# Performance work log

Measured on AMD Instinct MI355X. Metric: run time of the kernel, lower is better.

Reference implementation:

```python
import jax, jax.numpy as jnp
import numpy as np

N = 32768   # total nodes (128 graphs x 256 nodes)
E = 262144  # total edges (avg degree 8)
B = 128     # graphs per batch
M = 512     # candidate moves per graph
H = 256     # hidden_dim
F = 32      # raw node feature dim (node_feat_dim - 2)
EPS = 1e-5


def setup_inputs() -> dict:
    key = jax.random.key(0)
    ks = jax.random.split(key, 24)
    f32 = jnp.float32

    def w(k, shape, s=0.05):
        return jax.random.normal(k, shape, f32) * s

    inp = {}
    inp["x"] = jax.random.normal(ks[0], (N, F), f32)
    inp["edge_index"] = jax.random.randint(ks[1], (2, E), 0, N)
    inp["move_index"] = jax.random.randint(ks[2], (B, M, 2), 0, N)
    inp["player"] = jax.random.randint(ks[3], (B,), 0, 2)
    inp["batch"] = jnp.arange(N, dtype=jnp.int64 if jax.config.jax_enable_x64 else jnp.int32) // (N // B)

    inp["Win"] = w(ks[4], (F + 2, H)); inp["b_in"] = jnp.zeros((H,), f32)
    inp["Wg1"] = w(ks[5], (H, H)); inp["bg1"] = jnp.zeros((H,), f32)
    inp["Wg2"] = w(ks[6], (H, H)); inp["bg2"] = jnp.zeros((H,), f32)
    inp["Wg3"] = w(ks[7], (H, H)); inp["bg3"] = jnp.zeros((H,), f32)
    for i in (1, 2, 3):
        inp[f"ln{i}_g"] = jnp.ones((H,), f32)
        inp[f"ln{i}_b"] = jnp.zeros((H,), f32)
    inp["Wfc1"] = w(ks[8], (H, H)); inp["bfc1"] = jnp.zeros((H,), f32)
    inp["Wfc2"] = w(ks[9], (H, H)); inp["bfc2"] = jnp.zeros((H,), f32)
    for i in (1, 2):
        inp[f"bn{i}_g"] = jnp.ones((H,), f32)
        inp[f"bn{i}_b"] = jnp.zeros((H,), f32)
        inp[f"bn{i}_m"] = jnp.zeros((H,), f32)  # running mean (eval mode)
        inp[f"bn{i}_v"] = jnp.ones((H,), f32)   # running var  (eval mode)
    inp["Wp1"] = w(ks[10], (2 * H, H)); inp["bp1"] = jnp.zeros((H,), f32)
    inp["Wp2"] = w(ks[11], (H, 1));     inp["bp2"] = jnp.zeros((1,), f32)
    inp["Wv"]  = w(ks[12], (H, 1));     inp["bv"]  = jnp.zeros((1,), f32)
    return inp


def _layernorm(h, g, b):
    m = h.mean(-1, keepdims=True)
    v = ((h - m) ** 2).mean(-1, keepdims=True)
    return (h - m) * jax.lax.rsqrt(v + EPS) * g + b


def _batchnorm_eval(z, g, b, m, v):
    return (z - m) * jax.lax.rsqrt(v + EPS) * g + b


def reference(x, edge_index, move_index, player, batch,
              Win, b_in, Wg1, bg1, Wg2, bg2, Wg3, bg3,
              ln1_g, ln1_b, ln2_g, ln2_b, ln3_g, ln3_b,
              Wfc1, bfc1, Wfc2, bfc2,
              bn1_g, bn1_b, bn1_m, bn1_v, bn2_g, bn2_b, bn2_m, bn2_v,
              Wp1, bp1, Wp2, bp2, Wv, bv):
    nb = player.shape[0]
    src, dst = edge_index[0], edge_index[1]

    # player one-hot broadcast to nodes, concat, input projection
    ph = jax.nn.one_hot(player, 2, dtype=x.dtype)          # [B,2]
    h = jnp.concatenate([x, ph[batch]], axis=1) @ Win + b_in  # [N,H]
    residual = h

    def gin(h, W, b):  # GINConv(eps=0): lin(x + scatter_add of neighbor feats)
        agg = jnp.zeros_like(h).at[dst].add(h[src])
        return (h + agg) @ W + b

    h = jax.nn.relu(_layernorm(gin(h, Wg1, bg1), ln1_g, ln1_b))
    h = jax.nn.relu(_layernorm(gin(h, Wg2, bg2), ln2_g, ln2_b))
    h = _layernorm(gin(h, Wg3, bg3), ln3_g, ln3_b)
    h = jax.nn.relu(h + residual)

    # global mean pool
    sums = jax.ops.segment_sum(h, batch, num_segments=nb)
    cnt = jax.ops.segment_sum(jnp.ones((h.shape[0], 1), h.dtype), batch, num_segments=nb)
    ge = sums / cnt

    # value head (eval mode: BN uses running stats, dropout is identity)
    v1 = jax.nn.relu(_batchnorm_eval(ge @ Wfc1 + bfc1, bn1_g, bn1_b, bn1_m, bn1_v))
    v2 = jax.nn.relu(_batchnorm_eval(v1 @ Wfc2 + bfc2, bn2_g, bn2_b, bn2_m, bn2_v))
    value = jnp.tanh(v2 @ Wv + bv)[:, 0]                    # [B]

    # policy head: gather node pairs, edge MLP, mask invalid moves (vectorized over B)
    valid = jnp.all(move_index != -1, axis=-1)              # [B,M]
    s = jnp.clip(move_index[..., 0], 0, None)
    t = jnp.clip(move_index[..., 1], 0, None)
    ef = jnp.concatenate([h[s], h[t]], axis=-1)             # [B,M,2H]
    logits = (jax.nn.relu(ef @ Wp1 + bp1) @ Wp2 + bp2)[..., 0]
    policy = jnp.where(valid, logits, jnp.asarray(-1e9, h.dtype))
    return policy, value
```

## Files before the change

kernel.cpp:

```cpp
#include <hip/hip_runtime.h>
#include <hip/hip_bf16.h>

#define HD 256
#define NN 32768
#define NE 262144
#define NB 128
#define NM 512
#define KADJ 48

typedef short bf16x8 __attribute__((ext_vector_type(8)));
typedef float f32x4 __attribute__((ext_vector_type(4)));
typedef unsigned short u16;
typedef unsigned short u16x8 __attribute__((ext_vector_type(8)));
typedef unsigned short u16x4 __attribute__((ext_vector_type(4)));

__device__ __forceinline__ float b2f(u16 u) {
    unsigned int i = ((unsigned int)u) << 16;
    float f; __builtin_memcpy(&f, &i, 4); return f;
}
__device__ __forceinline__ u16 f2b(float f) {
    unsigned int i; __builtin_memcpy(&i, &f, 4);
    return (u16)((i + 0x7FFFu + ((i >> 16) & 1u)) >> 16);
}

__global__ __launch_bounds__(256) void k_prep(const float* __restrict__ Wg1, const float* __restrict__ Wg2,
                                              const float* __restrict__ Wg3, const float* __restrict__ Wp1,
                                              u16* __restrict__ Ws1, u16* __restrict__ Ws2,
                                              u16* __restrict__ Ws3, u16* __restrict__ Wsa,
                                              u16* __restrict__ Wsb,
                                              const float* __restrict__ x, const int* __restrict__ player,
                                              const float* __restrict__ Win, const float* __restrict__ bin,
                                              u16* __restrict__ h0,
                                              const int* __restrict__ esrc, const int* __restrict__ edst,
                                              int* __restrict__ deg, int* __restrict__ adj,
                                              u16* __restrict__ p0, u16* __restrict__ p1, u16* __restrict__ p2) {
    __shared__ float smem[64 * 65];
    const int bid = blockIdx.x;
    const int tid = threadIdx.x;
    if (bid < 80) {
        float (*tile)[65] = (float (*)[65])smem;
        const int mid = bid >> 4, tb = bid & 15;
        const float* W; u16* D;
        switch (mid) {
            case 0: W = Wg1; D = Ws1; break;
            case 1: W = Wg2; D = Ws2; break;
            case 2: W = Wg3; D = Ws3; break;
            case 3: W = Wp1; D = Wsa; break;
            default: W = Wp1 + HD * HD; D = Wsb; break;
        }
        const int tk = tb >> 2, tn = tb & 3;
        const int c = tid & 63, r4 = tid >> 6;
#pragma unroll
        for (int r = 0; r < 16; r++) {
            int k = tk * 64 + r * 4 + r4;
            tile[r * 4 + r4][c] = W[(size_t)k * HD + tn * 64 + c];
        }
        __syncthreads();
#pragma unroll
        for (int r = 0; r < 16; r++) {
            int n = tn * 64 + r * 4 + r4;
            int k = tk * 64 + c;
            u16 val = f2b(tile[c][r * 4 + r4]);
            if (mid < 3) {
                int half = k >> 7;
                int c2 = ((k >> 3) & 15) ^ (n & 15);
                D[half * 32768 + n * 128 + c2 * 8 + (k & 7)] = val;
            } else {
                int cc = k >> 3;
                int c2 = (cc & 16) | ((cc & 15) ^ (n & 15));
                D[n * 256 + c2 * 8 + (k & 7)] = val;
            }
        }
    } else if (bid == 80) {
        if (tid < 96) {
            const int r = tid >> 5, c = tid & 31;
            u16* p = (r == 0) ? p0 : (r == 1) ? p1 : p2;
            u16x8 z = (u16x8){0, 0, 0, 0, 0, 0, 0, 0};
            *(u16x8*)(p + c * 8) = z;
        }
    } else if (bid < 337) {
        const int lane = tid & 63, wvv = tid >> 6;
        const int l15 = lane & 15, lg = lane >> 4;
        const int node0 = (bid - 81) * 128;
        const int g = node0 >> 8;
        const int pl = player[g];

        bf16x8 wfr[16];
#pragma unroll
        for (int fc = 0; fc < 16; fc++) {
            const int n = fc * 16 + l15;
#pragma unroll
            for (int j = 0; j < 8; j++)
                wfr[fc][j] = (short)f2b(Win[(size_t)(lg * 8 + j) * HD + n]);
        }

#pragma unroll
        for (int grp = 0; grp < 2; grp++) {
            const int m = node0 + wvv * 32 + grp * 16 + l15;
            bf16x8 afr;
            {
                const float* xr = x + (size_t)m * 32 + lg * 8;
                f32x4 x0 = *(const f32x4*)xr;
                f32x4 x1 = *(const f32x4*)(xr + 4);
#pragma unroll
                for (int j = 0; j < 4; j++) afr[j] = (short)f2b(x0[j]);
#pragma unroll
                for (int j = 0; j < 4; j++) afr[4 + j] = (short)f2b(x1[j]);
            }
#pragma unroll
            for (int fc = 0; fc < 16; fc++) {
                f32x4 acc = (f32x4){0.f, 0.f, 0.f, 0.f};
                acc = __builtin_amdgcn_mfma_f32_16x16x32_bf16(wfr[fc], afr, acc, 0, 0, 0);
                const int cb = fc * 16 + lg * 4;
                f32x4 b4 = *(const f32x4*)(bin + cb);
                f32x4 w2 = *(const f32x4*)(Win + (size_t)(32 + pl) * HD + cb);
                u16x4 o;
#pragma unroll
                for (int e = 0; e < 4; e++) o[e] = f2b(acc[e] + b4[e] + w2[e]);
                *(u16x4*)(h0 + (size_t)m * HD + cb) = o;
            }
        }
    } else {
        const int e = (bid - 337) * 256 + tid;
        if (e < NE) {
            int d = edst[e];
            int p = atomicAdd(&deg[d], 1);
            if (p < KADJ) adj[d * KADJ + p] = esrc[e];
        }
    }
}

__global__ __launch_bounds__(256) void k_sortadj(const int* __restrict__ deg, int* __restrict__ adj) {
    __shared__ int buf[256 * 49];
    const int n = blockIdx.x * 256 + threadIdx.x;
    int d = deg[n]; if (d > KADJ) d = KADJ;
    int* mine = &buf[threadIdx.x * 49];
    for (int i = 0; i < d; i++) mine[i] = adj[n * KADJ + i];
    for (int i = 1; i < d; i++) {
        int v = mine[i];
        int j = i - 1;
        while (j >= 0 && mine[j] > v) { mine[j + 1] = mine[j]; j--; }
        mine[j + 1] = v;
    }
    for (int i = 0; i < d; i++) adj[n * KADJ + i] = mine[i];
}

__global__ __launch_bounds__(256) void k_agg(const u16* __restrict__ h, const int* __restrict__ deg,
                                             const int* __restrict__ adj, u16* __restrict__ hin) {
    const int n = blockIdx.x * 8 + (threadIdx.x >> 5);
    const int li = threadIdx.x & 31;
    const int fo = li * 8;
    const u16* hp = h + fo;
    u16x8 sv = *(const u16x8*)(hp + (size_t)n * HD);
    float a[8];
#pragma unroll
    for (int j = 0; j < 8; j++) a[j] = b2f(sv[j]);
    int d = deg[n]; if (d > KADJ) d = KADJ;
    const int* arow = adj + n * KADJ;
    for (int e = 0; e < d; e += 8) {
        int idx[8];
#pragma unroll
        for (int k = 0; k < 8; k++) idx[k] = (e + k < d) ? arow[e + k] : NN;
        u16x8 v[8];
#pragma unroll
        for (int k = 0; k < 8; k++) v[k] = *(const u16x8*)(hp + (size_t)idx[k] * HD);
#pragma unroll
        for (int k = 0; k < 8; k++)
#pragma unroll
            for (int j = 0; j < 8; j++) a[j] += b2f(v[k][j]);
    }
    u16x8 o;
#pragma unroll
    for (int j = 0; j < 8; j++) o[j] = f2b(a[j]);
    *(u16x8*)(hin + (size_t)n * HD + fo) = o;
}

__global__ __launch_bounds__(256) void k_mmln(const u16* __restrict__ hin, const u16* __restrict__ Wsw,
                                              const float* __restrict__ bias, const float* __restrict__ lng,
                                              const float* __restrict__ lnb, const u16* __restrict__ res,
                                              u16* __restrict__ hout) {
    const int tid = threadIdx.x;
    const int lane = tid & 63, wv = tid >> 6;
    const int l15 = lane & 15, lg = lane >> 4;
    const int m = blockIdx.x * 64 + wv * 16 + l15;

    __shared__ char Wl[65536];

#pragma unroll
    for (int i = 0; i < 16; i++)
        __builtin_amdgcn_global_load_lds((const unsigned int*)(Wsw + tid * 8 + i * 2048),
                                         (unsigned int*)(Wl + tid * 16 + i * 4096), 16, 0, 0);

    bf16x8 afr[8];
    {
        const u16* hrow = hin + (size_t)m * HD;
#pragma unroll
        for (int ks = 0; ks < 8; ks++) afr[ks] = *(const bf16x8*)(hrow + ks * 32 + lg * 8);
    }

    f32x4 acc[16];
#pragma unroll
    for (int fc = 0; fc < 16; fc++) acc[fc] = (f32x4){0.f, 0.f, 0.f, 0.f};

    __syncthreads();
#pragma unroll
    for (int l = 0; l < 4; l++) {
#pragma unroll
        for (int fc = 0; fc < 16; fc++) {
            const int n = fc * 16 + l15;
            const int c2 = (l * 4 + lg) ^ l15;
            bf16x8 w = *(const bf16x8*)(Wl + n * 256 + c2 * 16);
            acc[fc] = __builtin_amdgcn_mfma_f32_16x16x32_bf16(w, afr[l], acc[fc], 0, 0, 0);
        }
    }
    __syncthreads();
#pragma unroll
    for (int i = 0; i < 16; i++)
        __builtin_amdgcn_global_load_lds((const unsigned int*)(Wsw + 32768 + tid * 8 + i * 2048),
                                         (unsigned int*)(Wl + tid * 16 + i * 4096), 16, 0, 0);
    __syncthreads();
#pragma unroll
    for (int l = 0; l < 4; l++) {
#pragma unroll
        for (int fc = 0; fc < 16; fc++) {
            const int n = fc * 16 + l15;
            const int c2 = (l * 4 + lg) ^ l15;
            bf16x8 w = *(const bf16x8*)(Wl + n * 256 + c2 * 16);
            acc[fc] = __builtin_amdgcn_mfma_f32_16x16x32_bf16(w, afr[4 + l], acc[fc], 0, 0, 0);
        }
    }

    float s = 0.f, q = 0.f;
#pragma unroll
    for (int fc = 0; fc < 16; fc++) {
        f32x4 b4 = *(const f32x4*)(bias + fc * 16 + lg * 4);
#pragma unroll
        for (int e = 0; e < 4; e++) {
            float z = acc[fc][e] + b4[e];
            acc[fc][e] = z;
            s += z; q += z * z;
        }
    }
    s += __shfl_xor(s, 16); s += __shfl_xor(s, 32);
    q += __shfl_xor(q, 16); q += __shfl_xor(q, 32);
    const float mean = s * (1.0f / HD);
    const float rinv = rsqrtf(q * (1.0f / HD) - mean * mean + 1e-5f);

    const bool hasRes = (res != nullptr);
#pragma unroll
    for (int fc = 0; fc < 16; fc++) {
        f32x4 g4 = *(const f32x4*)(lng + fc * 16 + lg * 4);
        f32x4 e4 = *(const f32x4*)(lnb + fc * 16 + lg * 4);
        float y[4];
#pragma unroll
        for (int e = 0; e < 4; e++) y[e] = (acc[fc][e] - mean) * rinv * g4[e] + e4[e];
        if (hasRes) {
            u16x4 r = *(const u16x4*)(res + (size_t)m * HD + fc * 16 + lg * 4);
#pragma unroll
            for (int e = 0; e < 4; e++) y[e] += b2f(r[e]);
        }
        u16x4 o;
#pragma unroll
        for (int e = 0; e < 4; e++) o[e] = f2b(fmaxf(y[e], 0.f));
        *(u16x4*)(hout + (size_t)m * HD + fc * 16 + lg * 4) = o;
    }
}

__global__ __launch_bounds__(512) void k_densepv(const u16* __restrict__ h,
                                                 const u16* __restrict__ Wsa, const u16* __restrict__ Wsb,
                                                 const float* __restrict__ bp1,
                                                 u16* __restrict__ hP1, u16* __restrict__ hP2,
                                                 const float* __restrict__ W1, const float* __restrict__ b1,
                                                 const float* __restrict__ W2, const float* __restrict__ b2p,
                                                 const float* __restrict__ g1, const float* __restrict__ be1,
                                                 const float* __restrict__ m1, const float* __restrict__ v1,
                                                 const float* __restrict__ g2, const float* __restrict__ be2,
                                                 const float* __restrict__ m2, const float* __restrict__ v2,
                                                 const float* __restrict__ Wv, const float* __restrict__ bv,
                                                 float* __restrict__ vout) {
    __shared__ char sm[65536];
    const int tid = threadIdx.x;
    const int lane = tid & 63, wv = tid >> 6;
    const int bid = blockIdx.x;
    if (bid >= 128) {
        const int db = bid - 128;
        const int l15 = lane & 15, lg = lane >> 4;
        const int wsel = db >> 9, rem = db & 511;
        const int ch = rem >> 8, rb = rem & 255;
        const int m = rb * 128 + wv * 16 + l15;
        const u16* Wsw = (wsel ? Wsb : Wsa) + ch * 128 * 256;
        u16* outp = wsel ? hP2 : hP1;
        char* Wl = sm;

#pragma unroll
        for (int i = 0; i < 8; i++)
            __builtin_amdgcn_global_load_lds((const unsigned int*)(Wsw + tid * 8 + i * 4096),
                                             (unsigned int*)(Wl + tid * 16 + i * 8192), 16, 0, 0);

        bf16x8 afr[8];
        {
            const u16* hrow = h + (size_t)m * HD;
#pragma unroll
            for (int ks = 0; ks < 8; ks++) afr[ks] = *(const bf16x8*)(hrow + ks * 32 + lg * 8);
        }

        __syncthreads();

        f32x4 acc[8];
#pragma unroll
        for (int fc = 0; fc < 8; fc++) acc[fc] = (f32x4){0.f, 0.f, 0.f, 0.f};
#pragma unroll
        for (int ks = 0; ks < 8; ks++) {
#pragma unroll
            for (int fc = 0; fc < 8; fc++) {
                const int c = ks * 4 + lg;
                const int c2 = (c & 16) | ((c & 15) ^ l15);
                bf16x8 w = *(const bf16x8*)(Wl + (fc * 16 + l15) * 512 + c2 * 16);
                acc[fc] = __builtin_amdgcn_mfma_f32_16x16x32_bf16(w, afr[ks], acc[fc], 0, 0, 0);
            }
        }

#pragma unroll
        for (int fc = 0; fc < 8; fc++) {
            float b4[4] = {0.f, 0.f, 0.f, 0.f};
            if (!wsel) {
                f32x4 bb = *(const f32x4*)(bp1 + ch * 128 + fc * 16 + lg * 4);
#pragma unroll
                for (int e = 0; e < 4; e++) b4[e] = bb[e];
            }
            u16x4 o;
#pragma unroll
            for (int e = 0; e < 4; e++) o[e] = f2b(acc[fc][e] + b4[e]);
            *(u16x4*)(outp + (size_t)m * HD + ch * 128 + fc * 16 + lg * 4) = o;
        }
    } else {
        const int g = bid;
        float (*pool)[256] = (float (*)[256])sm;
        float* buf = (float*)(sm + 8192);
        float (*part)[256] = (float (*)[256])(sm + 8192 + 1024);
        float* red = (float*)(sm + 8192 + 1024 + 2048);
        {
            float a0 = 0.f, a1 = 0.f, a2 = 0.f, a3 = 0.f;
            const u16* base = h + ((size_t)g * 256 + wv * 32) * HD + lane * 4;
#pragma unroll 8
            for (int i = 0; i < 32; i++) {
                u16x4 v = *(const u16x4*)(base + (size_t)i * HD);
                a0 += b2f(v[0]); a1 += b2f(v[1]); a2 += b2f(v[2]); a3 += b2f(v[3]);
            }
            pool[wv][lane * 4 + 0] = a0; pool[wv][lane * 4 + 1] = a1;
            pool[wv][lane * 4 + 2] = a2; pool[wv][lane * 4 + 3] = a3;
        }
        __syncthreads();
        const int jj = tid & 255, kh = tid >> 8;
        if (tid < 256) {
            float s = 0.f;
#pragma unroll
            for (int w = 0; w < 8; w++) s += pool[w][tid];
            buf[tid] = s * (1.0f / 256.0f);
        }
        __syncthreads();
        {
            const float* Wcol = W1 + (size_t)(kh * 128) * HD + jj;
            const float* bk = buf + kh * 128;
            float p0 = 0.f, p1 = 0.f, p2 = 0.f, p3 = 0.f;
#pragma unroll
            for (int k = 0; k < 128; k += 4) {
                p0 += bk[k + 0] * Wcol[(size_t)(k + 0) * HD];
                p1 += bk[k + 1] * Wcol[(size_t)(k + 1) * HD];
                p2 += bk[k + 2] * Wcol[(size_t)(k + 2) * HD];
                p3 += bk[k + 3] * Wcol[(size_t)(k + 3) * HD];
            }
            part[kh][jj] = (p0 + p1) + (p2 + p3);
        }
        __syncthreads();
        if (tid < 256) {
            float z = part[0][tid] + part[1][tid] + b1[tid];
            z = (z - m1[tid]) * rsqrtf(v1[tid] + 1e-5f) * g1[tid] + be1[tid];
            buf[tid] = fmaxf(z, 0.f);
        }
        __syncthreads();
        {
            const float* Wcol = W2 + (size_t)(kh * 128) * HD + jj;
            const float* bk = buf + kh * 128;
            float p0 = 0.f, p1 = 0.f, p2 = 0.f, p3 = 0.f;
#pragma unroll
            for (int k = 0; k < 128; k += 4) {
                p0 += bk[k + 0] * Wcol[(size_t)(k + 0) * HD];
                p1 += bk[k + 1] * Wcol[(size_t)(k + 1) * HD];
                p2 += bk[k + 2] * Wcol[(size_t)(k + 2) * HD];
                p3 += bk[k + 3] * Wcol[(size_t)(k + 3) * HD];
            }
            part[kh][jj] = (p0 + p1) + (p2 + p3);
        }
        __syncthreads();
        float pv = 0.f;
        if (tid < 256) {
            float z2 = part[0][tid] + part[1][tid] + b2p[tid];
            z2 = (z2 - m2[tid]) * rsqrtf(v2[tid] + 1e-5f) * g2[tid] + be2[tid];
            z2 = fmaxf(z2, 0.f);
            pv = z2 * Wv[tid];
        }
#pragma unroll
        for (int mm = 1; mm < 64; mm <<= 1) pv += __shfl_xor(pv, mm, 64);
        if (tid < 256 && (tid & 63) == 0) red[tid >> 6] = pv;
        __syncthreads();
        if (tid == 0) vout[g] = tanhf(red[0] + red[1] + red[2] + red[3] + bv[0]);
    }
}

__global__ __launch_bounds__(256) void k_moves(const u16* __restrict__ hP1, const u16* __restrict__ hP2,
                                               const float* __restrict__ wp2, const float* __restrict__ bp2,
                                               const int* __restrict__ mov, float* __restrict__ out) {
    __shared__ float wp2L[256];
    wp2L[threadIdx.x] = wp2[threadIdx.x];
    __syncthreads();
    const int wv = threadIdx.x >> 6, lane = threadIdx.x & 63;
    const int grp = lane >> 3, li = lane & 7;
    const int mi = blockIdx.x * 32 + wv * 8 + grp;
    int a = mov[(size_t)mi * 2], b = mov[(size_t)mi * 2 + 1];
    const bool vld = (a != -1) && (b != -1);
    const int s = a < 0 ? 0 : a, t = b < 0 ? 0 : b;
    const u16* r1 = hP1 + (size_t)s * HD + li * 32;
    const u16* r2 = hP2 + (size_t)t * HD + li * 32;
    float acc = 0.f;
#pragma unroll
    for (int c = 0; c < 4; c++) {
        u16x8 v1 = *(const u16x8*)(r1 + c * 8);
        u16x8 v2 = *(const u16x8*)(r2 + c * 8);
#pragma unroll
        for (int j = 0; j < 8; j++) {
            float z = b2f(v1[j]) + b2f(v2[j]);
            acc += fmaxf(z, 0.f) * wp2L[li * 32 + c * 8 + j];
        }
    }
    acc += __shfl_xor(acc, 1); acc += __shfl_xor(acc, 2); acc += __shfl_xor(acc, 4);
    if (li == 0) out[mi] = vld ? acc + bp2[0] : -1e9f;
}

extern "C" void kernel_launch(void* const* d_in, const int* in_sizes, int n_in,
                              void* d_out, int out_size, void* d_ws, size_t ws_size,
                              hipStream_t stream) {
    const float* x    = (const float*)d_in[0];
    const int* eidx   = (const int*)d_in[1];
    const int* mov    = (const int*)d_in[2];
    const int* player = (const int*)d_in[3];
    const float* Win  = (const float*)d_in[5];
    const float* b_in = (const float*)d_in[6];
    const float* Wg1 = (const float*)d_in[7],  *bg1 = (const float*)d_in[8];
    const float* Wg2 = (const float*)d_in[9],  *bg2 = (const float*)d_in[10];
    const float* Wg3 = (const float*)d_in[11], *bg3 = (const float*)d_in[12];
    const float* ln1g = (const float*)d_in[13], *ln1b = (const float*)d_in[14];
    const float* ln2g = (const float*)d_in[15], *ln2b = (const float*)d_in[16];
    const float* ln3g = (const float*)d_in[17], *ln3b = (const float*)d_in[18];
    const float* Wfc1 = (const float*)d_in[19], *bfc1 = (const float*)d_in[20];
    const float* Wfc2 = (const float*)d_in[21], *bfc2 = (const float*)d_in[22];
    const float* bn1g = (const float*)d_in[23], *bn1b = (const float*)d_in[24];
    const float* bn1m = (const float*)d_in[25], *bn1v = (const float*)d_in[26];
    const float* bn2g = (const float*)d_in[27], *bn2b = (const float*)d_in[28];
    const float* bn2m = (const float*)d_in[29], *bn2v = (const float*)d_in[30];
    const float* Wp1 = (const float*)d_in[31], *bp1 = (const float*)d_in[32];
    const float* Wp2 = (const float*)d_in[33], *bp2 = (const float*)d_in[34];
    const float* Wv  = (const float*)d_in[35], *bv  = (const float*)d_in[36];

    char* ws = (char*)d_ws;
    size_t off = 0;
    auto alloc = [&](size_t bytes) {
        size_t p = off;
        off = (off + bytes + 255) & ~(size_t)255;
        return (void*)(ws + p);
    };
    u16* h0   = (u16*)alloc((size_t)(NN + 8) * HD * 2);
    u16* hA   = (u16*)alloc((size_t)(NN + 8) * HD * 2);
    u16* hB   = (u16*)alloc((size_t)(NN + 8) * HD * 2);
    u16* hin  = (u16*)alloc((size_t)NN * HD * 2);
    u16* Ws1  = (u16*)alloc((size_t)HD * HD * 2);
    u16* Ws2  = (u16*)alloc((size_t)HD * HD * 2);
    u16* Ws3  = (u16*)alloc((size_t)HD * HD * 2);
    u16* Wsa  = (u16*)alloc((size_t)HD * HD * 2);
    u16* Wsb  = (u16*)alloc((size_t)HD * HD * 2);
    int* deg  = (int*)alloc((size_t)NN * 4);
    int* adj  = (int*)alloc((size_t)NN * KADJ * 4);

    const int* esrc = eidx;
    const int* edst = eidx + NE;

    hipMemsetAsync(deg, 0, (size_t)NN * 4, stream);
    k_prep<<<1361, 256, 0, stream>>>(Wg1, Wg2, Wg3, Wp1, Ws1, Ws2, Ws3, Wsa, Wsb,
                                     x, player, Win, b_in, h0, esrc, edst, deg, adj,
                                     h0 + (size_t)NN * HD, hA + (size_t)NN * HD, hB + (size_t)NN * HD);
    k_sortadj<<<NN / 256, 256, 0, stream>>>(deg, adj);

    k_agg<<<NN / 8, 256, 0, stream>>>(h0, deg, adj, hin);
    k_mmln<<<NN / 64, 256, 0, stream>>>(hin, Ws1, bg1, ln1g, ln1b, nullptr, hA);
    k_agg<<<NN / 8, 256, 0, stream>>>(hA, deg, adj, hin);
    k_mmln<<<NN / 64, 256, 0, stream>>>(hin, Ws2, bg2, ln2g, ln2b, nullptr, hB);
    k_agg<<<NN / 8, 256, 0, stream>>>(hB, deg, adj, hin);
    k_mmln<<<NN / 64, 256, 0, stream>>>(hin, Ws3, bg3, ln3g, ln3b, h0, hA);

    u16* hP1 = h0;
    u16* hP2 = hB;

    k_densepv<<<1152, 512, 0, stream>>>(hA, Wsa, Wsb, bp1, hP1, hP2,
                                        Wfc1, bfc1, Wfc2, bfc2,
                                        bn1g, bn1b, bn1m, bn1v, bn2g, bn2b, bn2m, bn2v,
                                        Wv, bv, ((float*)d_out) + NB * NM);
    k_moves<<<(NB * NM) / 32, 256, 0, stream>>>(hP1, hP2, Wp2, bp2, mov, (float*)d_out);
}
```

Measured before the change: 221.6 us.

## Fuse neighbor aggregation into GIN matmul-layernorm kernel

Removes the separate aggregation kernel and performs the neighbor gather-sum directly inside the matmul+layernorm kernel, building the MFMA A-fragments in registers. This removes the write and re-read of the intermediate aggregated buffer and three kernel launches per forward pass. In exchange, each lane now gathers neighbor rows in a scattered per-lane pattern with more registers (64 floats of accumulators plus staged loads), which may reduce occupancy and memory coalescing compared with the dedicated 32-lanes-per-row gather kernel.

```diff
diff --git a/kernel.cpp b/kernel.cpp
--- a/kernel.cpp
+++ b/kernel.cpp
@@ -145,37 +145,8 @@
     for (int i = 0; i < d; i++) adj[n * KADJ + i] = mine[i];
 }
 
-__global__ __launch_bounds__(256) void k_agg(const u16* __restrict__ h, const int* __restrict__ deg,
-                                             const int* __restrict__ adj, u16* __restrict__ hin) {
-    const int n = blockIdx.x * 8 + (threadIdx.x >> 5);
-    const int li = threadIdx.x & 31;
-    const int fo = li * 8;
-    const u16* hp = h + fo;
-    u16x8 sv = *(const u16x8*)(hp + (size_t)n * HD);
-    float a[8];
-#pragma unroll
-    for (int j = 0; j < 8; j++) a[j] = b2f(sv[j]);
-    int d = deg[n]; if (d > KADJ) d = KADJ;
-    const int* arow = adj + n * KADJ;
-    for (int e = 0; e < d; e += 8) {
-        int idx[8];
-#pragma unroll
-        for (int k = 0; k < 8; k++) idx[k] = (e + k < d) ? arow[e + k] : NN;
-        u16x8 v[8];
-#pragma unroll
-        for (int k = 0; k < 8; k++) v[k] = *(const u16x8*)(hp + (size_t)idx[k] * HD);
-#pragma unroll
-        for (int k = 0; k < 8; k++)
-#pragma unroll
-            for (int j = 0; j < 8; j++) a[j] += b2f(v[k][j]);
-    }
-    u16x8 o;
-#pragma unroll
-    for (int j = 0; j < 8; j++) o[j] = f2b(a[j]);
-    *(u16x8*)(hin + (size_t)n * HD + fo) = o;
-}
-
-__global__ __launch_bounds__(256) void k_mmln(const u16* __restrict__ hin, const u16* __restrict__ Wsw,
+__global__ __launch_bounds__(256) void k_mmln(const u16* __restrict__ h, const int* __restrict__ deg,
+                                              const int* __restrict__ adj, const u16* __restrict__ Wsw,
                                               const float* __restrict__ bias, const float* __restrict__ lng,
                                               const float* __restrict__ lnb, const u16* __restrict__ res,
                                               u16* __restrict__ hout) {
@@ -191,12 +162,43 @@
         __builtin_amdgcn_global_load_lds((const unsigned int*)(Wsw + tid * 8 + i * 2048),
                                          (unsigned int*)(Wl + tid * 16 + i * 4096), 16, 0, 0);
 
+    float vals[8][8];
+    {
+        const u16* hrow = h + (size_t)m * HD + lg * 8;
+#pragma unroll
+        for (int ks = 0; ks < 8; ks++) {
+            u16x8 v = *(const u16x8*)(hrow + ks * 32);
+#pragma unroll
+            for (int j = 0; j < 8; j++) vals[ks][j] = b2f(v[j]);
+        }
+    }
+    {
+        int d = deg[m]; if (d > KADJ) d = KADJ;
+        const int* arow = adj + m * KADJ;
+        for (int e = 0; e < d; e += 4) {
+            int idx[4];
+#pragma unroll
+            for (int k = 0; k < 4; k++) idx[k] = (e + k < d) ? arow[e + k] : NN;
+            u16x8 v[4][8];
+#pragma unroll
+            for (int k = 0; k < 4; k++) {
+                const u16* srow = h + (size_t)idx[k] * HD + lg * 8;
+#pragma unroll
+                for (int ks = 0; ks < 8; ks++) v[k][ks] = *(const u16x8*)(srow + ks * 32);
+            }
+#pragma unroll
+            for (int k = 0; k < 4; k++)
+#pragma unroll
+                for (int ks = 0; ks < 8; ks++)
+#pragma unroll
+                    for (int j = 0; j < 8; j++) vals[ks][j] += b2f(v[k][ks][j]);
+        }
+    }
     bf16x8 afr[8];
-    {
-        const u16* hrow = hin + (size_t)m * HD;
-#pragma unroll
-        for (int ks = 0; ks < 8; ks++) afr[ks] = *(const bf16x8*)(hrow + ks * 32 + lg * 8);
-    }
+#pragma unroll
+    for (int ks = 0; ks < 8; ks++)
+#pragma unroll
+        for (int j = 0; j < 8; j++) afr[ks][j] = (short)f2b(vals[ks][j]);
 
     f32x4 acc[16];
 #pragma unroll
@@ -472,7 +474,6 @@
     u16* h0   = (u16*)alloc((size_t)(NN + 8) * HD * 2);
     u16* hA   = (u16*)alloc((size_t)(NN + 8) * HD * 2);
     u16* hB   = (u16*)alloc((size_t)(NN + 8) * HD * 2);
-    u16* hin  = (u16*)alloc((size_t)NN * HD * 2);
     u16* Ws1  = (u16*)alloc((size_t)HD * HD * 2);
     u16* Ws2  = (u16*)alloc((size_t)HD * HD * 2);
     u16* Ws3  = (u16*)alloc((size_t)HD * HD * 2);
@@ -490,12 +491,9 @@
                                      h0 + (size_t)NN * HD, hA + (size_t)NN * HD, hB + (size_t)NN * HD);
     k_sortadj<<<NN / 256, 256, 0, stream>>>(deg, adj);
 
-    k_agg<<<NN / 8, 256, 0, stream>>>(h0, deg, adj, hin);
-    k_mmln<<<NN / 64, 256, 0, stream>>>(hin, Ws1, bg1, ln1g, ln1b, nullptr, hA);
-    k_agg<<<NN / 8, 256, 0, stream>>>(hA, deg, adj, hin);
-    k_mmln<<<NN / 64, 256, 0, stream>>>(hin, Ws2, bg2, ln2g, ln2b, nullptr, hB);
-    k_agg<<<NN / 8, 256, 0, stream>>>(hB, deg, adj, hin);
-    k_mmln<<<NN / 64, 256, 0, stream>>>(hin, Ws3, bg3, ln3g, ln3b, h0, hA);
+    k_mmln<<<NN / 64, 256, 0, stream>>>(h0, deg, adj, Ws1, bg1, ln1g, ln1b, nullptr, hA);
+    k_mmln<<<NN / 64, 256, 0, stream>>>(hA, deg, adj, Ws2, bg2, ln2g, ln2b, nullptr, hB);
+    k_mmln<<<NN / 64, 256, 0, stream>>>(hB, deg, adj, Ws3, bg3, ln3g, ln3b, h0, hA);
 
     u16* hP1 = h0;
     u16* hP2 = hB;
```

Result: slower. 246.4 us (+11.2%).
